# Kernel optimization log

Measured on AMD Instinct MI355X. Metric: run time of the kernel, lower is better.

Reference implementation:

```python
import jax, jax.numpy as jnp
import numpy as np

IN_CH = 512
EMB = 512

def setup_inputs() -> dict:
    key = jax.random.key(0)
    ks = jax.random.split(key, 14)
    s = 0.02
    inp = {
        'input': jax.random.normal(ks[0], (8, IN_CH, 64, 64), jnp.float32),
        'context': jax.random.normal(ks[1], (8, EMB, 32, 32), jnp.float32),
        # proj_in: Conv2d(in_channels, emb_dim, 1) -> weight [emb, in_ch]
        'proj_in_w': jax.random.normal(ks[2], (EMB, IN_CH), jnp.float32) * s,
        'proj_in_b': jnp.zeros((EMB,), jnp.float32),
        # Linear weights stored as [in, out] (math-equivalent to torch [out,in].T)
        'wq_w': jax.random.normal(ks[3], (EMB, EMB), jnp.float32) * s,
        'wq_b': jnp.zeros((EMB,), jnp.float32),
        'wk_w': jax.random.normal(ks[4], (EMB, EMB), jnp.float32) * s,
        'wk_b': jnp.zeros((EMB,), jnp.float32),
        'wv_w': jax.random.normal(ks[5], (EMB, EMB), jnp.float32) * s,
        'wv_b': jnp.zeros((EMB,), jnp.float32),
        # proj_out: Conv2d(emb+in_ch, in_ch, 1) -> weight [in_ch, emb+in_ch]
        'proj_out_w': jax.random.normal(ks[6], (IN_CH, EMB + IN_CH), jnp.float32) * s,
        'proj_out_b': jnp.zeros((IN_CH,), jnp.float32),
    }
    return inp

def reference(input, context, proj_in_w, proj_in_b, wq_w, wq_b, wk_w, wk_b,
              wv_w, wv_b, proj_out_w, proj_out_b):
    b, c_in, h, w = input.shape
    _, c_ctx, hc, wc = context.shape
    scale = EMB ** (-0.5)

    # context: [b, emb, hc, wc] -> [b, L, emb]
    ctx = context.reshape(b, c_ctx, hc * wc).transpose(0, 2, 1)

    # proj_in (1x1 conv) + flatten: [b, in_ch, h, w] -> [b, hw, emb]
    x = jnp.einsum('bchw,ec->bhwe', input, proj_in_w) + proj_in_b
    x = x.reshape(b, h * w, EMB)

    Q = x @ wq_w + wq_b                 # [b, hw, emb]
    K = ctx @ wk_w + wk_b               # [b, L, emb]
    V = ctx @ wv_w + wv_b               # [b, L, emb]

    att = jnp.einsum('bid,bjd->bij', Q, K) * scale  # [b, hw, L]
    att = jax.nn.softmax(att, axis=-1)
    out = jnp.einsum('bij,bjd->bid', att, V)        # [b, hw, emb]

    # [b, hw, emb] -> [b, emb, h, w]
    out = out.reshape(b, h, w, EMB).transpose(0, 3, 1, 2)
    out = jnp.concatenate([input, out], axis=1)     # [b, in_ch+emb, h, w]
    out = jnp.einsum('bchw,oc->bohw', out, proj_out_w) + proj_out_b[None, :, None, None]
    return out
```

## Files before the change

### kernel.cpp

```cpp
#include <hip/hip_runtime.h>
#include <hip/hip_bf16.h>

using bf16 = __hip_bfloat16;
typedef short s16x8 __attribute__((ext_vector_type(8)));
typedef float f32x4 __attribute__((ext_vector_type(4)));
typedef unsigned short u16;

__device__ __forceinline__ void gld_lds16(const void* g, void* l) {
  __builtin_amdgcn_global_load_lds(
      (const __attribute__((address_space(1))) void*)g,
      (__attribute__((address_space(3))) void*)l, 16, 0, 0);
}

__device__ __forceinline__ float bf2f(u16 u) {
  unsigned int x = ((unsigned int)u) << 16;
  return __builtin_bit_cast(float, x);
}

__global__ __launch_bounds__(256) void convert_f32_bf16(
    const float* __restrict__ in, bf16* __restrict__ out, int n) {
  int i = blockIdx.x * 256 + threadIdx.x;
  if (i < n) out[i] = __float2bfloat16(in[i]);
}

__global__ __launch_bounds__(256) void zero_f32(float* __restrict__ p, int n) {
  int i = blockIdx.x * 256 + threadIdx.x;
  if (i < n) p[i] = 0.f;
}

__global__ __launch_bounds__(256) void transpose_f32_to_bf16(
    const float* __restrict__ in, bf16* __restrict__ out, int inner,
    long in_b, long out_b, int out_ld, int coloff) {
  __shared__ float tile[32][33];
  const int bx = blockIdx.x;
  const int by = blockIdx.y;
  const int bz = blockIdx.z;
  const int tx = threadIdx.x & 31;
  const int ty = threadIdx.x >> 5;
  const float* ib = in + (long)bz * in_b;
  bf16* ob = out + (long)bz * out_b;
#pragma unroll
  for (int i = 0; i < 4; ++i) {
    int r = ty + i * 8;
    tile[r][tx] = ib[(long)(by * 32 + r) * inner + bx * 32 + tx];
  }
  __syncthreads();
#pragma unroll
  for (int i = 0; i < 4; ++i) {
    int r = ty + i * 8;
    ob[(long)(bx * 32 + r) * out_ld + coloff + by * 32 + tx] =
        __float2bfloat16(tile[tx][r]);
  }
}

__global__ __launch_bounds__(256) void bias_combine(
    const float* __restrict__ pb, const float* __restrict__ wq,
    const float* __restrict__ qb, float* __restrict__ out) {
  int o = blockIdx.x * 256 + threadIdx.x;
  if (o >= 512) return;
  float s = qb[o];
  for (int e = 0; e < 512; ++e) s += pb[e] * wq[e * 512 + o];
  out[o] = s;
}

template <int OUT_BF16, int BIAS_MODE, int EPI>
__global__ __launch_bounds__(256, 4) void gemm_bt_kernel(
    const bf16* __restrict__ A, long sAb, int lda,
    const bf16* __restrict__ B, long sBb, int ldb,
    void* __restrict__ Cp, long sCb, int ldc,
    const float* __restrict__ bias, float* __restrict__ sc, long scb,
    float alpha, int K, int lgx, int lgy) {
  __shared__ __align__(16) bf16 tA[128 * 64];
  __shared__ __align__(16) bf16 tB[128 * 64];

  const int nwg = gridDim.x;
  const int orig = blockIdx.x;
  const int q = nwg >> 3, r = nwg & 7;
  const int xcd = orig & 7, local = orig >> 3;
  const int wgid = (xcd < r ? xcd * (q + 1) : r * (q + 1) + (xcd - r) * q) + local;
  const int bn = wgid & ((1 << lgx) - 1);
  const int tmp = wgid >> lgx;
  const int bm = tmp & ((1 << lgy) - 1);
  const int bz = tmp >> lgy;

  const int t = threadIdx.x;
  const int w = t >> 6;
  const int lane = t & 63;

  const bf16* Ab = A + (long)bz * sAb;
  const bf16* Bb = B + (long)bz * sBb;

  const int srow = t >> 3;
  const int schunk = (t & 7) ^ (srow & 7);
  const int scol = schunk * 8;
  const long a_base = (long)(bm * 128 + srow) * lda + scol;
  const long b_base = (long)(bn * 128 + srow) * ldb + scol;
  char* lA = (char*)tA + w * 1024;
  char* lB = (char*)tB + w * 1024;

  const int wr = w >> 1, wc = w & 1;
  const int r15 = lane & 15;
  const int khalf = lane >> 4;
  f32x4 acc[4][4] = {};

  for (int kt = 0; kt < K; kt += 64) {
#pragma unroll
    for (int i = 0; i < 4; ++i) {
      gld_lds16(Ab + a_base + (long)(i * 32) * lda + kt, lA + i * 4096);
      gld_lds16(Bb + b_base + (long)(i * 32) * ldb + kt, lB + i * 4096);
    }
    __syncthreads();
#pragma unroll
    for (int kk = 0; kk < 2; ++kk) {
      const int chunk = kk * 4 + khalf;
      s16x8 af[4], bg[4];
#pragma unroll
      for (int m = 0; m < 4; ++m) {
        const int row = wr * 64 + m * 16 + r15;
        af[m] = *(const s16x8*)(tA + row * 64 + ((chunk ^ (row & 7)) * 8));
      }
#pragma unroll
      for (int n = 0; n < 4; ++n) {
        const int row = wc * 64 + n * 16 + r15;
        bg[n] = *(const s16x8*)(tB + row * 64 + ((chunk ^ (row & 7)) * 8));
      }
#pragma unroll
      for (int m = 0; m < 4; ++m)
#pragma unroll
        for (int n = 0; n < 4; ++n)
          acc[m][n] = __builtin_amdgcn_mfma_f32_16x16x32_bf16(af[m], bg[n],
                                                              acc[m][n], 0, 0, 0);
    }
    __syncthreads();
  }

#pragma unroll
  for (int m = 0; m < 4; ++m) {
    const int rb = bm * 128 + wr * 64 + m * 16 + (lane >> 4) * 4;
    float rin[4];
    if (EPI == 2) {
#pragma unroll
      for (int j = 0; j < 4; ++j) rin[j] = 1.0f / sc[(long)bz * scb + rb + j];
    }
    float rs[4] = {0.f, 0.f, 0.f, 0.f};
#pragma unroll
    for (int n = 0; n < 4; ++n) {
      const int col = bn * 128 + wc * 64 + n * 16 + r15;
      float bN = 0.f;
      if (BIAS_MODE == 1) bN = bias[col];
#pragma unroll
      for (int j = 0; j < 4; ++j) {
        const int row = rb + j;
        float v;
        if (EPI == 1) {
          v = __expf(acc[m][n][j] * alpha);
          rs[j] += v;
        } else if (EPI == 2) {
          v = acc[m][n][j] * rin[j];
        } else {
          v = acc[m][n][j] * alpha;
          if (BIAS_MODE == 1) v += bN;
          if (BIAS_MODE == 2) v += bias[row];
        }
        const long off = (long)bz * sCb + (long)row * ldc + col;
        if (OUT_BF16)
          ((bf16*)Cp)[off] = __float2bfloat16(v);
        else
          ((float*)Cp)[off] = v;
      }
    }
    if (EPI == 1) {
#pragma unroll
      for (int j = 0; j < 4; ++j) {
        float s = rs[j];
#pragma unroll
        for (int sh = 1; sh < 16; sh <<= 1) s += __shfl_xor(s, sh, 64);
        if (r15 == 0) atomicAdd(sc + (long)bz * scb + rb + j, s);
      }
    }
  }
}

extern "C" void kernel_launch(void* const* d_in, const int* in_sizes, int n_in,
                              void* d_out, int out_size, void* d_ws, size_t ws_size,
                              hipStream_t stream) {
  const float* input   = (const float*)d_in[0];
  const float* context = (const float*)d_in[1];
  const float* pin_w   = (const float*)d_in[2];
  const float* pin_b   = (const float*)d_in[3];
  const float* wq_w    = (const float*)d_in[4];
  const float* wq_b    = (const float*)d_in[5];
  const float* wk_w    = (const float*)d_in[6];
  const float* wk_b    = (const float*)d_in[7];
  const float* wv_w    = (const float*)d_in[8];
  const float* wv_b    = (const float*)d_in[9];
  const float* pout_w  = (const float*)d_in[10];
  const float* pout_b  = (const float*)d_in[11];

  char* ws = (char*)d_ws;
  size_t off = 0;
  auto alloc = [&](size_t bytes) -> void* {
    void* p = ws + off;
    off += (bytes + 255) & ~(size_t)255;
    return p;
  };
  bf16* poutw = (bf16*)alloc((size_t)512 * 1024 * 2);
  bf16* wqT  = (bf16*)alloc((size_t)512 * 512 * 2);
  bf16* wkT  = (bf16*)alloc((size_t)512 * 512 * 2);
  bf16* wvT  = (bf16*)alloc((size_t)512 * 512 * 2);
  bf16* pinT = (bf16*)alloc((size_t)512 * 512 * 2);
  bf16* WQc  = (bf16*)alloc((size_t)512 * 512 * 2);
  float* bQc = (float*)alloc((size_t)512 * 4);
  bf16* cat  = (bf16*)alloc((size_t)32768 * 1024 * 2);
  bf16* ctxt = (bf16*)alloc((size_t)8192 * 512 * 2);
  bf16* Qb   = (bf16*)alloc((size_t)32768 * 512 * 2);
  bf16* Kmb  = (bf16*)alloc((size_t)8192 * 512 * 2);
  bf16* Vtb  = (bf16*)alloc((size_t)8 * 512 * 1024 * 2);
  bf16* Sb   = (bf16*)alloc((size_t)8 * 4096 * 1024 * 2);
  float* rsum = (float*)alloc((size_t)32768 * 4);

  dim3 blk(256);

  convert_f32_bf16<<<2048, blk, 0, stream>>>(pout_w, poutw, 512 * 1024);
  zero_f32<<<128, blk, 0, stream>>>(rsum, 32768);
  transpose_f32_to_bf16<<<dim3(16, 16, 1), blk, 0, stream>>>(wq_w, wqT, 512, 0, 0, 512, 0);
  transpose_f32_to_bf16<<<dim3(16, 16, 1), blk, 0, stream>>>(wk_w, wkT, 512, 0, 0, 512, 0);
  transpose_f32_to_bf16<<<dim3(16, 16, 1), blk, 0, stream>>>(wv_w, wvT, 512, 0, 0, 512, 0);
  transpose_f32_to_bf16<<<dim3(16, 16, 1), blk, 0, stream>>>(pin_w, pinT, 512, 0, 0, 512, 0);
  bias_combine<<<2, blk, 0, stream>>>(pin_b, wq_w, wq_b, bQc);
  transpose_f32_to_bf16<<<dim3(128, 16, 8), blk, 0, stream>>>(
      input, cat, 4096, (long)512 * 4096, (long)4096 * 1024, 1024, 0);
  transpose_f32_to_bf16<<<dim3(32, 16, 8), blk, 0, stream>>>(
      context, ctxt, 1024, (long)512 * 1024, (long)1024 * 512, 512, 0);

  const float scale = 0.04419417382415922f;

  gemm_bt_kernel<1, 0, 0><<<dim3(16), blk, 0, stream>>>(
      wqT, 0, 512, pinT, 0, 512, WQc, 0, 512, nullptr, nullptr, 0, 1.f, 512, 2, 2);
  gemm_bt_kernel<1, 1, 0><<<dim3(1024), blk, 0, stream>>>(
      cat, 0, 1024, WQc, 0, 512, Qb, 0, 512, bQc, nullptr, 0, 1.f, 512, 2, 8);
  gemm_bt_kernel<1, 1, 0><<<dim3(256), blk, 0, stream>>>(
      ctxt, 0, 512, wkT, 0, 512, Kmb, 0, 512, wk_b, nullptr, 0, 1.f, 512, 2, 6);
  gemm_bt_kernel<1, 2, 0><<<dim3(256), blk, 0, stream>>>(
      wvT, 0, 512, ctxt, (long)1024 * 512, 512, Vtb, (long)512 * 1024, 1024,
      wv_b, nullptr, 0, 1.f, 512, 3, 2);
  gemm_bt_kernel<1, 0, 1><<<dim3(2048), blk, 0, stream>>>(
      Qb, (long)4096 * 512, 512, Kmb, (long)1024 * 512, 512, Sb,
      (long)4096 * 1024, 1024, nullptr, rsum, 4096, scale, 512, 3, 5);
  gemm_bt_kernel<1, 0, 2><<<dim3(1024), blk, 0, stream>>>(
      Sb, (long)4096 * 1024, 1024, Vtb, (long)512 * 1024, 1024,
      (void*)(cat + 512), (long)4096 * 1024, 1024, nullptr, rsum, 4096, 1.f,
      1024, 2, 5);
  gemm_bt_kernel<0, 2, 0><<<dim3(1024), blk, 0, stream>>>(
      poutw, 0, 1024, cat, (long)4096 * 1024, 1024, d_out,
      (long)512 * 4096, 4096, pout_b, nullptr, 0, 1.f, 1024, 5, 2);
}
```

Measured before the change: 380.6 us.

## Add double-buffered 256x256 GEMM kernel for large matmuls and fuse weight transposes

Introduces a 512-thread GEMM kernel with 256x256 output tiles and two LDS buffers (128KB of dynamic shared memory), so the load of the next K-slice overlaps MFMA compute on the current one. The four large GEMMs (Q projection, QK^T with exp, softmax-normalised PV, and proj_out) now use it, which raises data reuse per tile. The four separate weight-transpose launches are merged into one launch. The cost is one workgroup per CU because of LDS use, higher register pressure from 32 accumulators per thread, and fewer workgroups per GEMM (256-512), which may leave some CUs idle on 256 CUs.

```diff
diff --git a/kernel.cpp b/kernel.cpp
--- a/kernel.cpp
+++ b/kernel.cpp
@@ -53,6 +53,35 @@
   }
 }
 
+__global__ __launch_bounds__(256) void transpose_w4(
+    const float* __restrict__ w0, const float* __restrict__ w1,
+    const float* __restrict__ w2, const float* __restrict__ w3,
+    bf16* __restrict__ o0, bf16* __restrict__ o1,
+    bf16* __restrict__ o2, bf16* __restrict__ o3) {
+  __shared__ float tile[32][33];
+  const float* in;
+  bf16* out;
+  switch (blockIdx.z) {
+    case 0: in = w0; out = o0; break;
+    case 1: in = w1; out = o1; break;
+    case 2: in = w2; out = o2; break;
+    default: in = w3; out = o3; break;
+  }
+  const int bx = blockIdx.x, by = blockIdx.y;
+  const int tx = threadIdx.x & 31, ty = threadIdx.x >> 5;
+#pragma unroll
+  for (int i = 0; i < 4; ++i) {
+    int r = ty + i * 8;
+    tile[r][tx] = in[(long)(by * 32 + r) * 512 + bx * 32 + tx];
+  }
+  __syncthreads();
+#pragma unroll
+  for (int i = 0; i < 4; ++i) {
+    int r = ty + i * 8;
+    out[(long)(bx * 32 + r) * 512 + by * 32 + tx] = __float2bfloat16(tile[tx][r]);
+  }
+}
+
 __global__ __launch_bounds__(256) void bias_combine(
     const float* __restrict__ pb, const float* __restrict__ wq,
     const float* __restrict__ qb, float* __restrict__ out) {
@@ -91,8 +120,7 @@
   const bf16* Bb = B + (long)bz * sBb;
 
   const int srow = t >> 3;
-  const int schunk = (t & 7) ^ (srow & 7);
-  const int scol = schunk * 8;
+  const int scol = ((t & 7) ^ (srow & 7)) * 8;
   const long a_base = (long)(bm * 128 + srow) * lda + scol;
   const long b_base = (long)(bn * 128 + srow) * ldb + scol;
   char* lA = (char*)tA + w * 1024;
@@ -146,6 +174,143 @@
 #pragma unroll
     for (int n = 0; n < 4; ++n) {
       const int col = bn * 128 + wc * 64 + n * 16 + r15;
+      float bN = 0.f;
+      if (BIAS_MODE == 1) bN = bias[col];
+#pragma unroll
+      for (int j = 0; j < 4; ++j) {
+        const int row = rb + j;
+        float v;
+        if (EPI == 1) {
+          v = __expf(acc[m][n][j] * alpha);
+          rs[j] += v;
+        } else if (EPI == 2) {
+          v = acc[m][n][j] * rin[j];
+        } else {
+          v = acc[m][n][j] * alpha;
+          if (BIAS_MODE == 1) v += bN;
+          if (BIAS_MODE == 2) v += bias[row];
+        }
+        const long off = (long)bz * sCb + (long)row * ldc + col;
+        if (OUT_BF16)
+          ((bf16*)Cp)[off] = __float2bfloat16(v);
+        else
+          ((float*)Cp)[off] = v;
+      }
+    }
+    if (EPI == 1) {
+#pragma unroll
+      for (int j = 0; j < 4; ++j) {
+        float s = rs[j];
+#pragma unroll
+        for (int sh = 1; sh < 16; sh <<= 1) s += __shfl_xor(s, sh, 64);
+        if (r15 == 0) atomicAdd(sc + (long)bz * scb + rb + j, s);
+      }
+    }
+  }
+}
+
+template <int OUT_BF16, int BIAS_MODE, int EPI>
+__global__ __launch_bounds__(512) void gemm256_kernel(
+    const bf16* __restrict__ A, long sAb, int lda,
+    const bf16* __restrict__ B, long sBb, int ldb,
+    void* __restrict__ Cp, long sCb, int ldc,
+    const float* __restrict__ bias, float* __restrict__ sc, long scb,
+    float alpha, int K, int lgx, int lgy) {
+  extern __shared__ __align__(16) char smem[];
+  bf16* tA = (bf16*)smem;
+  bf16* tB = (bf16*)(smem + 65536);
+
+  const int nwg = gridDim.x;
+  const int orig = blockIdx.x;
+  const int q = nwg >> 3, r = nwg & 7;
+  const int xcd = orig & 7, local = orig >> 3;
+  const int wgid = (xcd < r ? xcd * (q + 1) : r * (q + 1) + (xcd - r) * q) + local;
+  const int bn = wgid & ((1 << lgx) - 1);
+  const int tmp = wgid >> lgx;
+  const int bm = tmp & ((1 << lgy) - 1);
+  const int bz = tmp >> lgy;
+
+  const int t = threadIdx.x;
+  const int w = t >> 6;
+  const int lane = t & 63;
+  const int wr = w >> 2, wc = w & 3;
+  const int r15 = lane & 15;
+  const int khalf = lane >> 4;
+
+  const bf16* Ab = A + (long)bz * sAb;
+  const bf16* Bb = B + (long)bz * sBb;
+
+  const int srow = t >> 3;
+  const int scol = ((t & 7) ^ (srow & 7)) * 8;
+  const long a_base = (long)(bm * 256 + srow) * lda + scol;
+  const long b_base = (long)(bn * 256 + srow) * ldb + scol;
+
+  f32x4 acc[8][4] = {};
+
+  auto STAGE = [&](int buf, int kt) {
+    char* dA = (char*)(tA + buf * 16384) + w * 1024;
+    char* dB = (char*)(tB + buf * 16384) + w * 1024;
+#pragma unroll
+    for (int i = 0; i < 4; ++i)
+      gld_lds16(Ab + a_base + (long)(i * 64) * lda + kt, dA + i * 8192);
+#pragma unroll
+    for (int i = 0; i < 4; ++i)
+      gld_lds16(Bb + b_base + (long)(i * 64) * ldb + kt, dB + i * 8192);
+  };
+
+  auto COMPUTE = [&](int buf) {
+    const bf16* tAc = tA + buf * 16384;
+    const bf16* tBc = tB + buf * 16384;
+    s16x8 bg[2][4];
+#pragma unroll
+    for (int ks = 0; ks < 2; ++ks)
+#pragma unroll
+      for (int n = 0; n < 4; ++n) {
+        const int row = wc * 64 + n * 16 + r15;
+        bg[ks][n] =
+            *(const s16x8*)(tBc + row * 64 + (((ks * 4 + khalf) ^ (row & 7)) * 8));
+      }
+#pragma unroll
+    for (int m = 0; m < 8; ++m) {
+      const int row = wr * 128 + m * 16 + r15;
+      const s16x8 a0 =
+          *(const s16x8*)(tAc + row * 64 + ((khalf ^ (row & 7)) * 8));
+      const s16x8 a1 =
+          *(const s16x8*)(tAc + row * 64 + (((4 + khalf) ^ (row & 7)) * 8));
+#pragma unroll
+      for (int n = 0; n < 4; ++n)
+        acc[m][n] =
+            __builtin_amdgcn_mfma_f32_16x16x32_bf16(a0, bg[0][n], acc[m][n], 0, 0, 0);
+#pragma unroll
+      for (int n = 0; n < 4; ++n)
+        acc[m][n] =
+            __builtin_amdgcn_mfma_f32_16x16x32_bf16(a1, bg[1][n], acc[m][n], 0, 0, 0);
+    }
+  };
+
+  STAGE(0, 0);
+  __syncthreads();
+  int cur = 0;
+  for (int kt = 64; kt < K; kt += 64) {
+    STAGE(cur ^ 1, kt);
+    COMPUTE(cur);
+    __syncthreads();
+    cur ^= 1;
+  }
+  COMPUTE(cur);
+
+#pragma unroll
+  for (int m = 0; m < 8; ++m) {
+    const int rb = bm * 256 + wr * 128 + m * 16 + (lane >> 4) * 4;
+    float rin[4];
+    if (EPI == 2) {
+#pragma unroll
+      for (int j = 0; j < 4; ++j) rin[j] = 1.0f / sc[(long)bz * scb + rb + j];
+    }
+    float rs[4] = {0.f, 0.f, 0.f, 0.f};
+#pragma unroll
+    for (int n = 0; n < 4; ++n) {
+      const int col = bn * 256 + wc * 64 + n * 16 + r15;
       float bN = 0.f;
       if (BIAS_MODE == 1) bN = bias[col];
 #pragma unroll
@@ -221,12 +386,19 @@
 
   dim3 blk(256);
 
+  hipFuncSetAttribute((const void*)gemm256_kernel<1, 1, 0>,
+                      hipFuncAttributeMaxDynamicSharedMemorySize, 131072);
+  hipFuncSetAttribute((const void*)gemm256_kernel<1, 0, 1>,
+                      hipFuncAttributeMaxDynamicSharedMemorySize, 131072);
+  hipFuncSetAttribute((const void*)gemm256_kernel<1, 0, 2>,
+                      hipFuncAttributeMaxDynamicSharedMemorySize, 131072);
+  hipFuncSetAttribute((const void*)gemm256_kernel<0, 2, 0>,
+                      hipFuncAttributeMaxDynamicSharedMemorySize, 131072);
+
   convert_f32_bf16<<<2048, blk, 0, stream>>>(pout_w, poutw, 512 * 1024);
   zero_f32<<<128, blk, 0, stream>>>(rsum, 32768);
-  transpose_f32_to_bf16<<<dim3(16, 16, 1), blk, 0, stream>>>(wq_w, wqT, 512, 0, 0, 512, 0);
-  transpose_f32_to_bf16<<<dim3(16, 16, 1), blk, 0, stream>>>(wk_w, wkT, 512, 0, 0, 512, 0);
-  transpose_f32_to_bf16<<<dim3(16, 16, 1), blk, 0, stream>>>(wv_w, wvT, 512, 0, 0, 512, 0);
-  transpose_f32_to_bf16<<<dim3(16, 16, 1), blk, 0, stream>>>(pin_w, pinT, 512, 0, 0, 512, 0);
+  transpose_w4<<<dim3(16, 16, 4), blk, 0, stream>>>(wq_w, wk_w, wv_w, pin_w,
+                                                    wqT, wkT, wvT, pinT);
   bias_combine<<<2, blk, 0, stream>>>(pin_b, wq_w, wq_b, bQc);
   transpose_f32_to_bf16<<<dim3(128, 16, 8), blk, 0, stream>>>(
       input, cat, 4096, (long)512 * 4096, (long)4096 * 1024, 1024, 0);
@@ -237,21 +409,22 @@
 
   gemm_bt_kernel<1, 0, 0><<<dim3(16), blk, 0, stream>>>(
       wqT, 0, 512, pinT, 0, 512, WQc, 0, 512, nullptr, nullptr, 0, 1.f, 512, 2, 2);
-  gemm_bt_kernel<1, 1, 0><<<dim3(1024), blk, 0, stream>>>(
-      cat, 0, 1024, WQc, 0, 512, Qb, 0, 512, bQc, nullptr, 0, 1.f, 512, 2, 8);
   gemm_bt_kernel<1, 1, 0><<<dim3(256), blk, 0, stream>>>(
       ctxt, 0, 512, wkT, 0, 512, Kmb, 0, 512, wk_b, nullptr, 0, 1.f, 512, 2, 6);
   gemm_bt_kernel<1, 2, 0><<<dim3(256), blk, 0, stream>>>(
       wvT, 0, 512, ctxt, (long)1024 * 512, 512, Vtb, (long)512 * 1024, 1024,
       wv_b, nullptr, 0, 1.f, 512, 3, 2);
-  gemm_bt_kernel<1, 0, 1><<<dim3(2048), blk, 0, stream>>>(
+
+  gemm256_kernel<1, 1, 0><<<dim3(256), dim3(512), 131072, stream>>>(
+      cat, 0, 1024, WQc, 0, 512, Qb, 0, 512, bQc, nullptr, 0, 1.f, 512, 1, 7);
+  gemm256_kernel<1, 0, 1><<<dim3(512), dim3(512), 131072, stream>>>(
       Qb, (long)4096 * 512, 512, Kmb, (long)1024 * 512, 512, Sb,
-      (long)4096 * 1024, 1024, nullptr, rsum, 4096, scale, 512, 3, 5);
-  gemm_bt_kernel<1, 0, 2><<<dim3(1024), blk, 0, stream>>>(
+      (long)4096 * 1024, 1024, nullptr, rsum, 4096, scale, 512, 2, 4);
+  gemm256_kernel<1, 0, 2><<<dim3(256), dim3(512), 131072, stream>>>(
       Sb, (long)4096 * 1024, 1024, Vtb, (long)512 * 1024, 1024,
       (void*)(cat + 512), (long)4096 * 1024, 1024, nullptr, rsum, 4096, 1.f,
-      1024, 2, 5);
-  gemm_bt_kernel<0, 2, 0><<<dim3(1024), blk, 0, stream>>>(
+      1024, 1, 4);
+  gemm256_kernel<0, 2, 0><<<dim3(256), dim3(512), 131072, stream>>>(
       poutw, 0, 1024, cat, (long)4096 * 1024, 1024, d_out,
-      (long)512 * 4096, 4096, pout_b, nullptr, 0, 1.f, 1024, 5, 2);
-}
+      (long)512 * 4096, 4096, pout_b, nullptr, 0, 1.f, 1024, 4, 1);
+}
```

Result: faster. 365.6 us (-3.9%).

## Fold V projection into proj_out weights and fuse attention-output GEMM with proj_out

Applied to the files above, without the earlier changes.

Precomputes Wv2 = proj_out_w[:,512:] · Wv, so V is projected straight into output space. The separate attn@V GEMM, which wrote bf16 into a concat buffer, is replaced by a fused kernel. That kernel accumulates S·Vt2 over K=1024, scales by the softmax reciprocal per output column, then accumulates proj_out_w[:, :512]·input over K=512 and adds a folded bias. This removes one full GEMM pass and the concat buffer round trip, and it halves the input transpose buffer. In exchange, the bf16 rounding point of the combined weight changes, and weight transposes are batched into a single kernel.

```diff
diff --git a/kernel.cpp b/kernel.cpp
--- a/kernel.cpp
+++ b/kernel.cpp
@@ -12,11 +12,6 @@
       (__attribute__((address_space(3))) void*)l, 16, 0, 0);
 }
 
-__device__ __forceinline__ float bf2f(u16 u) {
-  unsigned int x = ((unsigned int)u) << 16;
-  return __builtin_bit_cast(float, x);
-}
-
 __global__ __launch_bounds__(256) void convert_f32_bf16(
     const float* __restrict__ in, bf16* __restrict__ out, int n) {
   int i = blockIdx.x * 256 + threadIdx.x;
@@ -30,7 +25,7 @@
 
 __global__ __launch_bounds__(256) void transpose_f32_to_bf16(
     const float* __restrict__ in, bf16* __restrict__ out, int inner,
-    long in_b, long out_b, int out_ld, int coloff) {
+    long in_b, long out_b, int out_ld) {
   __shared__ float tile[32][33];
   const int bx = blockIdx.x;
   const int by = blockIdx.y;
@@ -48,8 +43,35 @@
 #pragma unroll
   for (int i = 0; i < 4; ++i) {
     int r = ty + i * 8;
-    ob[(long)(bx * 32 + r) * out_ld + coloff + by * 32 + tx] =
+    ob[(long)(bx * 32 + r) * out_ld + by * 32 + tx] =
         __float2bfloat16(tile[tx][r]);
+  }
+}
+
+__global__ __launch_bounds__(256) void transpose_w3(
+    const float* __restrict__ w0, const float* __restrict__ w1,
+    const float* __restrict__ w2,
+    bf16* __restrict__ o0, bf16* __restrict__ o1, bf16* __restrict__ o2) {
+  __shared__ float tile[32][33];
+  const float* in;
+  bf16* out;
+  switch (blockIdx.z) {
+    case 0: in = w0; out = o0; break;
+    case 1: in = w1; out = o1; break;
+    default: in = w2; out = o2; break;
+  }
+  const int bx = blockIdx.x, by = blockIdx.y;
+  const int tx = threadIdx.x & 31, ty = threadIdx.x >> 5;
+#pragma unroll
+  for (int i = 0; i < 4; ++i) {
+    int r = ty + i * 8;
+    tile[r][tx] = in[(long)(by * 32 + r) * 512 + bx * 32 + tx];
+  }
+  __syncthreads();
+#pragma unroll
+  for (int i = 0; i < 4; ++i) {
+    int r = ty + i * 8;
+    out[(long)(bx * 32 + r) * 512 + by * 32 + tx] = __float2bfloat16(tile[tx][r]);
   }
 }
 
@@ -60,6 +82,17 @@
   if (o >= 512) return;
   float s = qb[o];
   for (int e = 0; e < 512; ++e) s += pb[e] * wq[e * 512 + o];
+  out[o] = s;
+}
+
+__global__ __launch_bounds__(256) void bias_out(
+    const float* __restrict__ poutw, const float* __restrict__ wvb,
+    const float* __restrict__ pob, float* __restrict__ out) {
+  int o = blockIdx.x * 256 + threadIdx.x;
+  if (o >= 512) return;
+  float s = pob[o];
+  const float* row = poutw + (long)o * 1024 + 512;
+  for (int e = 0; e < 512; ++e) s += row[e] * wvb[e];
   out[o] = s;
 }
 
@@ -91,8 +124,7 @@
   const bf16* Bb = B + (long)bz * sBb;
 
   const int srow = t >> 3;
-  const int schunk = (t & 7) ^ (srow & 7);
-  const int scol = schunk * 8;
+  const int scol = ((t & 7) ^ (srow & 7)) * 8;
   const long a_base = (long)(bm * 128 + srow) * lda + scol;
   const long b_base = (long)(bn * 128 + srow) * ldb + scol;
   char* lA = (char*)tA + w * 1024;
@@ -137,11 +169,6 @@
 #pragma unroll
   for (int m = 0; m < 4; ++m) {
     const int rb = bm * 128 + wr * 64 + m * 16 + (lane >> 4) * 4;
-    float rin[4];
-    if (EPI == 2) {
-#pragma unroll
-      for (int j = 0; j < 4; ++j) rin[j] = 1.0f / sc[(long)bz * scb + rb + j];
-    }
     float rs[4] = {0.f, 0.f, 0.f, 0.f};
 #pragma unroll
     for (int n = 0; n < 4; ++n) {
@@ -155,8 +182,6 @@
         if (EPI == 1) {
           v = __expf(acc[m][n][j] * alpha);
           rs[j] += v;
-        } else if (EPI == 2) {
-          v = acc[m][n][j] * rin[j];
         } else {
           v = acc[m][n][j] * alpha;
           if (BIAS_MODE == 1) v += bN;
@@ -176,6 +201,138 @@
 #pragma unroll
         for (int sh = 1; sh < 16; sh <<= 1) s += __shfl_xor(s, sh, 64);
         if (r15 == 0) atomicAdd(sc + (long)bz * scb + rb + j, s);
+      }
+    }
+  }
+}
+
+__global__ __launch_bounds__(256, 4) void gemm_out_kernel(
+    const bf16* __restrict__ A2, const bf16* __restrict__ B2,
+    const bf16* __restrict__ A1, const bf16* __restrict__ B1,
+    float* __restrict__ C, const float* __restrict__ rsum,
+    const float* __restrict__ bias2) {
+  __shared__ __align__(16) bf16 tA[128 * 64];
+  __shared__ __align__(16) bf16 tB[128 * 64];
+
+  const int nwg = gridDim.x;
+  const int orig = blockIdx.x;
+  const int q = nwg >> 3, r = nwg & 7;
+  const int xcd = orig & 7, local = orig >> 3;
+  const int wgid = (xcd < r ? xcd * (q + 1) : r * (q + 1) + (xcd - r) * q) + local;
+  const int bn = wgid & 31;
+  const int tmp = wgid >> 5;
+  const int bm = tmp & 3;
+  const int bz = tmp >> 2;
+
+  const int t = threadIdx.x;
+  const int w = t >> 6;
+  const int lane = t & 63;
+
+  const int srow = t >> 3;
+  const int scol = ((t & 7) ^ (srow & 7)) * 8;
+  char* lA = (char*)tA + w * 1024;
+  char* lB = (char*)tB + w * 1024;
+
+  const int wr = w >> 1, wc = w & 1;
+  const int r15 = lane & 15;
+  const int khalf = lane >> 4;
+  f32x4 acc[4][4] = {};
+
+  {
+    const bf16* Ab = A2 + (long)bz * (512 * 1024);
+    const bf16* Bb = B2 + (long)bz * ((long)4096 * 1024);
+    const long a_base = (long)(bm * 128 + srow) * 1024 + scol;
+    const long b_base = (long)(bn * 128 + srow) * 1024 + scol;
+    for (int kt = 0; kt < 1024; kt += 64) {
+#pragma unroll
+      for (int i = 0; i < 4; ++i) {
+        gld_lds16(Ab + a_base + (long)(i * 32) * 1024 + kt, lA + i * 4096);
+        gld_lds16(Bb + b_base + (long)(i * 32) * 1024 + kt, lB + i * 4096);
+      }
+      __syncthreads();
+#pragma unroll
+      for (int kk = 0; kk < 2; ++kk) {
+        const int chunk = kk * 4 + khalf;
+        s16x8 af[4], bg[4];
+#pragma unroll
+        for (int m = 0; m < 4; ++m) {
+          const int row = wr * 64 + m * 16 + r15;
+          af[m] = *(const s16x8*)(tA + row * 64 + ((chunk ^ (row & 7)) * 8));
+        }
+#pragma unroll
+        for (int n = 0; n < 4; ++n) {
+          const int row = wc * 64 + n * 16 + r15;
+          bg[n] = *(const s16x8*)(tB + row * 64 + ((chunk ^ (row & 7)) * 8));
+        }
+#pragma unroll
+        for (int m = 0; m < 4; ++m)
+#pragma unroll
+          for (int n = 0; n < 4; ++n)
+            acc[m][n] = __builtin_amdgcn_mfma_f32_16x16x32_bf16(
+                af[m], bg[n], acc[m][n], 0, 0, 0);
+      }
+      __syncthreads();
+    }
+  }
+
+#pragma unroll
+  for (int n = 0; n < 4; ++n) {
+    const int col = bn * 128 + wc * 64 + n * 16 + r15;
+    const float rin = 1.0f / rsum[(long)bz * 4096 + col];
+#pragma unroll
+    for (int m = 0; m < 4; ++m)
+#pragma unroll
+      for (int j = 0; j < 4; ++j) acc[m][n][j] *= rin;
+  }
+
+  {
+    const bf16* Ab = A1;
+    const bf16* Bb = B1 + (long)bz * ((long)4096 * 512);
+    const long a_base = (long)(bm * 128 + srow) * 1024 + scol;
+    const long b_base = (long)(bn * 128 + srow) * 512 + scol;
+    for (int kt = 0; kt < 512; kt += 64) {
+#pragma unroll
+      for (int i = 0; i < 4; ++i) {
+        gld_lds16(Ab + a_base + (long)(i * 32) * 1024 + kt, lA + i * 4096);
+        gld_lds16(Bb + b_base + (long)(i * 32) * 512 + kt, lB + i * 4096);
+      }
+      __syncthreads();
+#pragma unroll
+      for (int kk = 0; kk < 2; ++kk) {
+        const int chunk = kk * 4 + khalf;
+        s16x8 af[4], bg[4];
+#pragma unroll
+        for (int m = 0; m < 4; ++m) {
+          const int row = wr * 64 + m * 16 + r15;
+          af[m] = *(const s16x8*)(tA + row * 64 + ((chunk ^ (row & 7)) * 8));
+        }
+#pragma unroll
+        for (int n = 0; n < 4; ++n) {
+          const int row = wc * 64 + n * 16 + r15;
+          bg[n] = *(const s16x8*)(tB + row * 64 + ((chunk ^ (row & 7)) * 8));
+        }
+#pragma unroll
+        for (int m = 0; m < 4; ++m)
+#pragma unroll
+          for (int n = 0; n < 4; ++n)
+            acc[m][n] = __builtin_amdgcn_mfma_f32_16x16x32_bf16(
+                af[m], bg[n], acc[m][n], 0, 0, 0);
+      }
+      __syncthreads();
+    }
+  }
+
+#pragma unroll
+  for (int m = 0; m < 4; ++m) {
+    const int rb = bm * 128 + wr * 64 + m * 16 + (lane >> 4) * 4;
+#pragma unroll
+    for (int n = 0; n < 4; ++n) {
+      const int col = bn * 128 + wc * 64 + n * 16 + r15;
+#pragma unroll
+      for (int j = 0; j < 4; ++j) {
+        const int row = rb + j;
+        C[(long)bz * (512L * 4096) + (long)row * 4096 + col] =
+            acc[m][n][j] + bias2[row];
       }
     }
   }
@@ -205,53 +362,53 @@
     return p;
   };
   bf16* poutw = (bf16*)alloc((size_t)512 * 1024 * 2);
+  bf16* wvC  = (bf16*)alloc((size_t)512 * 512 * 2);
   bf16* wqT  = (bf16*)alloc((size_t)512 * 512 * 2);
   bf16* wkT  = (bf16*)alloc((size_t)512 * 512 * 2);
-  bf16* wvT  = (bf16*)alloc((size_t)512 * 512 * 2);
   bf16* pinT = (bf16*)alloc((size_t)512 * 512 * 2);
   bf16* WQc  = (bf16*)alloc((size_t)512 * 512 * 2);
+  bf16* Wv2  = (bf16*)alloc((size_t)512 * 512 * 2);
   float* bQc = (float*)alloc((size_t)512 * 4);
-  bf16* cat  = (bf16*)alloc((size_t)32768 * 1024 * 2);
+  float* bO  = (float*)alloc((size_t)512 * 4);
+  bf16* catL = (bf16*)alloc((size_t)32768 * 512 * 2);
   bf16* ctxt = (bf16*)alloc((size_t)8192 * 512 * 2);
   bf16* Qb   = (bf16*)alloc((size_t)32768 * 512 * 2);
   bf16* Kmb  = (bf16*)alloc((size_t)8192 * 512 * 2);
-  bf16* Vtb  = (bf16*)alloc((size_t)8 * 512 * 1024 * 2);
+  bf16* Vt2  = (bf16*)alloc((size_t)8 * 512 * 1024 * 2);
   bf16* Sb   = (bf16*)alloc((size_t)8 * 4096 * 1024 * 2);
   float* rsum = (float*)alloc((size_t)32768 * 4);
 
   dim3 blk(256);
 
   convert_f32_bf16<<<2048, blk, 0, stream>>>(pout_w, poutw, 512 * 1024);
+  convert_f32_bf16<<<1024, blk, 0, stream>>>(wv_w, wvC, 512 * 512);
   zero_f32<<<128, blk, 0, stream>>>(rsum, 32768);
-  transpose_f32_to_bf16<<<dim3(16, 16, 1), blk, 0, stream>>>(wq_w, wqT, 512, 0, 0, 512, 0);
-  transpose_f32_to_bf16<<<dim3(16, 16, 1), blk, 0, stream>>>(wk_w, wkT, 512, 0, 0, 512, 0);
-  transpose_f32_to_bf16<<<dim3(16, 16, 1), blk, 0, stream>>>(wv_w, wvT, 512, 0, 0, 512, 0);
-  transpose_f32_to_bf16<<<dim3(16, 16, 1), blk, 0, stream>>>(pin_w, pinT, 512, 0, 0, 512, 0);
+  transpose_w3<<<dim3(16, 16, 3), blk, 0, stream>>>(wq_w, wk_w, pin_w,
+                                                    wqT, wkT, pinT);
   bias_combine<<<2, blk, 0, stream>>>(pin_b, wq_w, wq_b, bQc);
+  bias_out<<<2, blk, 0, stream>>>(pout_w, wv_b, pout_b, bO);
   transpose_f32_to_bf16<<<dim3(128, 16, 8), blk, 0, stream>>>(
-      input, cat, 4096, (long)512 * 4096, (long)4096 * 1024, 1024, 0);
+      input, catL, 4096, (long)512 * 4096, (long)4096 * 512, 512);
   transpose_f32_to_bf16<<<dim3(32, 16, 8), blk, 0, stream>>>(
-      context, ctxt, 1024, (long)512 * 1024, (long)1024 * 512, 512, 0);
+      context, ctxt, 1024, (long)512 * 1024, (long)1024 * 512, 512);
 
   const float scale = 0.04419417382415922f;
 
   gemm_bt_kernel<1, 0, 0><<<dim3(16), blk, 0, stream>>>(
       wqT, 0, 512, pinT, 0, 512, WQc, 0, 512, nullptr, nullptr, 0, 1.f, 512, 2, 2);
-  gemm_bt_kernel<1, 1, 0><<<dim3(1024), blk, 0, stream>>>(
-      cat, 0, 1024, WQc, 0, 512, Qb, 0, 512, bQc, nullptr, 0, 1.f, 512, 2, 8);
+  gemm_bt_kernel<1, 0, 0><<<dim3(16), blk, 0, stream>>>(
+      poutw + 512, 0, 1024, wvC, 0, 512, Wv2, 0, 512, nullptr, nullptr, 0, 1.f,
+      512, 2, 2);
   gemm_bt_kernel<1, 1, 0><<<dim3(256), blk, 0, stream>>>(
       ctxt, 0, 512, wkT, 0, 512, Kmb, 0, 512, wk_b, nullptr, 0, 1.f, 512, 2, 6);
-  gemm_bt_kernel<1, 2, 0><<<dim3(256), blk, 0, stream>>>(
-      wvT, 0, 512, ctxt, (long)1024 * 512, 512, Vtb, (long)512 * 1024, 1024,
-      wv_b, nullptr, 0, 1.f, 512, 3, 2);
+  gemm_bt_kernel<1, 0, 0><<<dim3(256), blk, 0, stream>>>(
+      Wv2, 0, 512, ctxt, (long)1024 * 512, 512, Vt2, (long)512 * 1024, 1024,
+      nullptr, nullptr, 0, 1.f, 512, 3, 2);
+  gemm_bt_kernel<1, 1, 0><<<dim3(1024), blk, 0, stream>>>(
+      catL, 0, 512, WQc, 0, 512, Qb, 0, 512, bQc, nullptr, 0, 1.f, 512, 2, 8);
   gemm_bt_kernel<1, 0, 1><<<dim3(2048), blk, 0, stream>>>(
       Qb, (long)4096 * 512, 512, Kmb, (long)1024 * 512, 512, Sb,
       (long)4096 * 1024, 1024, nullptr, rsum, 4096, scale, 512, 3, 5);
-  gemm_bt_kernel<1, 0, 2><<<dim3(1024), blk, 0, stream>>>(
-      Sb, (long)4096 * 1024, 1024, Vtb, (long)512 * 1024, 1024,
-      (void*)(cat + 512), (long)4096 * 1024, 1024, nullptr, rsum, 4096, 1.f,
-      1024, 2, 5);
-  gemm_bt_kernel<0, 2, 0><<<dim3(1024), blk, 0, stream>>>(
-      poutw, 0, 1024, cat, (long)4096 * 1024, 1024, d_out,
-      (long)512 * 4096, 4096, pout_b, nullptr, 0, 1.f, 1024, 5, 2);
-}
+  gemm_out_kernel<<<dim3(1024), blk, 0, stream>>>(
+      Vt2, Sb, poutw, catL, (float*)d_out, rsum, bO);
+}
```

Result: slower. 399.2 us (+4.9%).
